# Optimization experiments

Measured on AMD Instinct MI355X. Metric: run time of the kernel, lower is better.

The kernel has to match this reference:

```python
import jax, jax.numpy as jnp
import numpy as np

TAW = 0.02

def setup_inputs() -> dict:
    key = jax.random.key(0)
    k1, k2 = jax.random.split(key)
    query = jax.random.normal(k1, (8, 2048, 1024), dtype=jnp.float32)
    memory = jax.random.normal(k2, (8, 2048, 1024), dtype=jnp.float32)
    return {"query": query, "memory": memory}

def reference(query, memory):
    # scores: [B, Lq, Lkv]
    scores = jnp.einsum('bqd,bkd->bqk', query, memory) / TAW
    probs = jax.nn.softmax(scores, axis=-1)
    # out: [B, Lq, D]
    return jnp.einsum('bqk,bkd->bqd', probs, memory)
```

## Files before the change

### kernel.cpp

```cpp
#include <hip/hip_runtime.h>
#include <math.h>


typedef __bf16 bf16x8 __attribute__((ext_vector_type(8)));
typedef float  f32x4  __attribute__((ext_vector_type(4)));
typedef float  f32x16 __attribute__((ext_vector_type(16)));

constexpr int   B_    = 8;
constexpr int   L_    = 2048;
constexpr int   D_    = 1024;
constexpr float SCALE  = 50.0f;
constexpr float MARGIN = 1.2f;
constexpr int   BQ    = 64;
constexpr int   RCAP  = 64;

constexpr size_t WS_T_ELEMS = (size_t)8 * 64 * 2048 * 16;
constexpr size_t WS_NEED    = 2 * WS_T_ELEMS * 2;

static __device__ __forceinline__ unsigned short f2bf(float x) {
    unsigned u = __builtin_bit_cast(unsigned, x);
    u += 0x7FFFu + ((u >> 16) & 1u);
    return (unsigned short)(u >> 16);
}

__global__ __launch_bounds__(256) void convert_k(
    const float* __restrict__ Q, const float* __restrict__ M,
    __bf16* __restrict__ ws)
{
    const int t = blockIdx.y;
    const size_t g = (size_t)blockIdx.x * 256 + threadIdx.x;
    const int r    = (int)(g & 2047);
    const int dblk = (int)((g >> 11) & 63);
    const int b    = (int)(g >> 17);
    const float* src = (t ? M : Q) + ((size_t)b * L_ + r) * D_ + dblk * 16;
    __bf16* dst = ws + ((size_t)t * 8 + b) * (64ull * 2048 * 16)
                     + ((size_t)dblk * 2048 + r) * 16;
    union { unsigned short h[16]; uint4 u[2]; } o;
    #pragma unroll
    for (int c = 0; c < 4; ++c) {
        float4 v = ((const float4*)src)[c];
        o.h[c*4+0] = f2bf(v.x); o.h[c*4+1] = f2bf(v.y);
        o.h[c*4+2] = f2bf(v.z); o.h[c*4+3] = f2bf(v.w);
    }
    ((uint4*)dst)[0] = o.u[0];
    ((uint4*)dst)[1] = o.u[1];
}

__global__ __launch_bounds__(512, 2) void attn_main(
    const float* __restrict__ Q, const float* __restrict__ M,
    const __bf16* __restrict__ ws, float* __restrict__ Out)
{
    __shared__ float wmax[8][BQ];
    __shared__ float rm_s[BQ], thr_s[BQ];
    __shared__ int   rowcnt[BQ];
    __shared__ int   rowlist[BQ][RCAP];
    __shared__ float rowval[BQ][RCAP];

    const int b    = blockIdx.x & 7;
    const int qt   = blockIdx.x >> 3;
    const int q0   = qt * BQ;
    const int tid  = threadIdx.x;
    const int w    = tid >> 6;
    const int lane = tid & 63;
    const int ln31 = lane & 31;
    const int h2   = lane >> 5;

    const __bf16* qws = ws + (size_t)b * (64ull * 2048 * 16);
    const __bf16* mws = ws + ((size_t)8 + b) * (64ull * 2048 * 16);
    const float*  Qb  = Q + ((size_t)b * L_ + q0) * D_;
    const float*  Mb  = M + (size_t)b * L_ * D_;

    if (tid < BQ) { rm_s[tid] = -INFINITY; rowcnt[tid] = 0; }
    __syncthreads();

    #pragma unroll 1
    for (int kt = 0; kt < 2; ++kt) {
        const int nb = kt * 1024 + w * 128;

        f32x16 acc[2][4];
        #pragma unroll
        for (int i = 0; i < 2; ++i)
            #pragma unroll
            for (int j = 0; j < 4; ++j)
                #pragma unroll
                for (int e = 0; e < 16; ++e) acc[i][j][e] = 0.f;

        #pragma unroll 1
        for (int dq = 0; dq < 16; ++dq) {
            bf16x8 af[4][2], bf[4][4];
            #pragma unroll
            for (int ks = 0; ks < 4; ++ks) {
                const int dblk = dq * 4 + ks;
                const __bf16* qp = qws + ((size_t)dblk * 2048 + q0 + ln31) * 16 + h2 * 8;
                af[ks][0] = *(const bf16x8*)qp;
                af[ks][1] = *(const bf16x8*)(qp + 32 * 16);
                const __bf16* mp = mws + ((size_t)dblk * 2048 + nb + ln31) * 16 + h2 * 8;
                #pragma unroll
                for (int j = 0; j < 4; ++j)
                    bf[ks][j] = *(const bf16x8*)(mp + j * 32 * 16);
            }
            #pragma unroll
            for (int ks = 0; ks < 4; ++ks)
                #pragma unroll
                for (int i = 0; i < 2; ++i)
                    #pragma unroll
                    for (int j = 0; j < 4; ++j)
                        acc[i][j] = __builtin_amdgcn_mfma_f32_32x32x16_bf16(
                            af[ks][i], bf[ks][j], acc[i][j], 0, 0, 0);
        }

        float lm[2][16];
        #pragma unroll
        for (int i = 0; i < 2; ++i)
            #pragma unroll
            for (int g = 0; g < 16; ++g)
                lm[i][g] = fmaxf(fmaxf(acc[i][0][g], acc[i][1][g]),
                                 fmaxf(acc[i][2][g], acc[i][3][g]));
        #pragma unroll
        for (int off = 1; off <= 16; off <<= 1)
            #pragma unroll
            for (int i = 0; i < 2; ++i)
                #pragma unroll
                for (int g = 0; g < 16; ++g)
                    lm[i][g] = fmaxf(lm[i][g], __shfl_xor(lm[i][g], off, 64));
        if (ln31 == 0) {
            #pragma unroll
            for (int i = 0; i < 2; ++i)
                #pragma unroll
                for (int g = 0; g < 16; ++g)
                    wmax[w][i * 32 + (g & 3) + 8 * (g >> 2) + 4 * h2] = lm[i][g];
        }
        __syncthreads();
        if (tid < BQ) {
            float m = wmax[0][tid];
            #pragma unroll
            for (int ww = 1; ww < 8; ++ww) m = fmaxf(m, wmax[ww][tid]);
            m = fmaxf(m, rm_s[tid]);
            rm_s[tid] = m;
            thr_s[tid] = m - MARGIN;
        }
        __syncthreads();

        #pragma unroll
        for (int i = 0; i < 2; ++i)
            #pragma unroll
            for (int g = 0; g < 16; ++g) {
                const int rl = i * 32 + (g & 3) + 8 * (g >> 2) + 4 * h2;
                const float thr = thr_s[rl];
                #pragma unroll
                for (int j = 0; j < 4; ++j)
                    if (acc[i][j][g] > thr) {
                        int t = atomicAdd(&rowcnt[rl], 1);
                        if (t < RCAP) {
                            rowlist[rl][t] = nb + j * 32 + ln31;
                            rowval[rl][t]  = acc[i][j][g];
                        }
                    }
            }
    }
    __syncthreads();

    #pragma unroll 1
    for (int r = w; r < BQ; r += 8) {
        const int c = min(rowcnt[r], RCAP);
        const float thrf = rm_s[r] - MARGIN;
        #pragma unroll 1
        for (int t = 0; t < c; ++t) {
            const float av = rowval[r][t];
            if (av > thrf) {
                const int k = rowlist[r][t];
                const f32x4* qp = (const f32x4*)(Qb + (size_t)r * D_);
                const f32x4* mp = (const f32x4*)(Mb + (size_t)k * D_);
                float dot = 0.f;
                #pragma unroll
                for (int c4 = 0; c4 < 4; ++c4) {
                    f32x4 x = qp[lane + 64 * c4];
                    f32x4 y = mp[lane + 64 * c4];
                    dot += x[0]*y[0] + x[1]*y[1] + x[2]*y[2] + x[3]*y[3];
                }
                #pragma unroll
                for (int off = 32; off >= 1; off >>= 1)
                    dot += __shfl_xor(dot, off, 64);
                if (lane == 0) rowval[r][t] = dot;
            } else if (lane == 0) rowval[r][t] = -1e30f;
        }
    }
    __syncthreads();

    #pragma unroll 1
    for (int r = w; r < BQ; r += 8) {
        const int c = min(rowcnt[r], RCAP);
        float mstar = -1e30f;
        for (int t = 0; t < c; ++t) mstar = fmaxf(mstar, rowval[r][t]);
        float denom = 0.f;
        f32x4 o[4];
        #pragma unroll
        for (int c4 = 0; c4 < 4; ++c4) o[c4] = (f32x4){0.f, 0.f, 0.f, 0.f};
        #pragma unroll 1
        for (int t = 0; t < c; ++t) {
            const float wgt = __expf(SCALE * (rowval[r][t] - mstar));
            if (wgt > 1e-22f) {
                denom += wgt;
                const f32x4* mp = (const f32x4*)(Mb + (size_t)rowlist[r][t] * D_);
                #pragma unroll
                for (int c4 = 0; c4 < 4; ++c4)
                    o[c4] += mp[lane + 64 * c4] * wgt;
            }
        }
        const float inv = 1.f / denom;
        f32x4* op = (f32x4*)(Out + ((size_t)b * L_ + q0 + r) * D_);
        #pragma unroll
        for (int c4 = 0; c4 < 4; ++c4) op[lane + 64 * c4] = o[c4] * inv;
    }
}

constexpr int   FB_BKV  = 256;
constexpr int   FB_NKT  = L_ / FB_BKV;
constexpr int   FB_BD   = 32;
constexpr int   FB_NDC  = D_ / FB_BD;
constexpr int   FB_STR  = FB_BD + 8;
constexpr int   FB_CAP  = 2048;

__global__ __launch_bounds__(256) void attn_fb(
    const float* __restrict__ Q, const float* __restrict__ M,
    float* __restrict__ Out)
{
    __shared__ __bf16 qs[BQ * FB_STR];
    __shared__ __bf16 ms[FB_BKV * FB_STR];
    __shared__ float  wmax[4][BQ];
    __shared__ float  rowmax_s[BQ];
    __shared__ int    cnt_s;
    __shared__ int    list_s[FB_CAP];
    __shared__ float  elist_s[FB_CAP];

    const int b    = blockIdx.x & 7;
    const int qt   = blockIdx.x >> 3;
    const int q0   = qt * BQ;
    const int tid  = threadIdx.x;
    const int w    = tid >> 6;
    const int lane = tid & 63;
    const int ln15 = lane & 15;
    const int quad = lane >> 4;

    const float* Qb = Q + ((size_t)b * L_ + q0) * D_;
    const float* Mb = M + (size_t)b * L_ * D_;

    float rm[4][4];
    #pragma unroll
    for (int i = 0; i < 4; ++i)
        #pragma unroll
        for (int r = 0; r < 4; ++r) rm[i][r] = -INFINITY;

    #pragma unroll 1
    for (int pass = 0; pass < 2; ++pass) {
        #pragma unroll 1
        for (int kt = 0; kt < FB_NKT; ++kt) {
            f32x4 acc[4][4];
            #pragma unroll
            for (int i = 0; i < 4; ++i)
                #pragma unroll
                for (int j = 0; j < 4; ++j)
                    acc[i][j] = (f32x4){0.f, 0.f, 0.f, 0.f};
            const float* Mt = Mb + (size_t)(kt * FB_BKV) * D_;
            #pragma unroll 1
            for (int dc = 0; dc < FB_NDC; ++dc) {
                const int d0 = dc * FB_BD;
                __syncthreads();
                #pragma unroll
                for (int i = 0; i < 2; ++i) {
                    int f4 = tid + i * 256, row = f4 >> 3, c = f4 & 7;
                    float4 v = *(const float4*)(Qb + row * D_ + d0 + c * 4);
                    union { unsigned short h[4]; uint2 u; } t;
                    t.h[0] = f2bf(v.x); t.h[1] = f2bf(v.y);
                    t.h[2] = f2bf(v.z); t.h[3] = f2bf(v.w);
                    *(uint2*)(qs + row * FB_STR + c * 4) = t.u;
                }
                #pragma unroll
                for (int i = 0; i < 8; ++i) {
                    int f4 = tid + i * 256, row = f4 >> 3, c = f4 & 7;
                    float4 v = *(const float4*)(Mt + row * D_ + d0 + c * 4);
                    union { unsigned short h[4]; uint2 u; } t;
                    t.h[0] = f2bf(v.x); t.h[1] = f2bf(v.y);
                    t.h[2] = f2bf(v.z); t.h[3] = f2bf(v.w);
                    *(uint2*)(ms + row * FB_STR + c * 4) = t.u;
                }
                __syncthreads();
                bf16x8 afr[4], bfr[4];
                #pragma unroll
                for (int i = 0; i < 4; ++i)
                    afr[i] = *(const bf16x8*)(qs + (i * 16 + ln15) * FB_STR + quad * 8);
                #pragma unroll
                for (int j = 0; j < 4; ++j)
                    bfr[j] = *(const bf16x8*)(ms + (w * 64 + j * 16 + ln15) * FB_STR + quad * 8);
                #pragma unroll
                for (int i = 0; i < 4; ++i)
                    #pragma unroll
                    for (int j = 0; j < 4; ++j)
                        acc[i][j] = __builtin_amdgcn_mfma_f32_16x16x32_bf16(
                            afr[i], bfr[j], acc[i][j], 0, 0, 0);
            }
            if (pass == 0) {
                #pragma unroll
                for (int i = 0; i < 4; ++i)
                    #pragma unroll
                    for (int r = 0; r < 4; ++r) {
                        float m0 = fmaxf(fmaxf(acc[i][0][r], acc[i][1][r]),
                                         fmaxf(acc[i][2][r], acc[i][3][r]));
                        rm[i][r] = fmaxf(rm[i][r], m0);
                    }
            } else {
                #pragma unroll
                for (int i = 0; i < 4; ++i)
                    #pragma unroll
                    for (int j = 0; j < 4; ++j)
                        #pragma unroll
                        for (int r = 0; r < 4; ++r)
                            if (acc[i][j][r] > rm[i][r]) {
                                int idx = atomicAdd(&cnt_s, 1);
                                if (idx < FB_CAP)
                                    list_s[idx] = ((i * 16 + quad * 4 + r) << 16) |
                                                  (kt * FB_BKV + w * 64 + j * 16 + ln15);
                            }
            }
        }
        if (pass == 0) {
            #pragma unroll
            for (int i = 0; i < 4; ++i)
                #pragma unroll
                for (int r = 0; r < 4; ++r) {
                    float v = rm[i][r];
                    v = fmaxf(v, __shfl_xor(v, 1, 64));
                    v = fmaxf(v, __shfl_xor(v, 2, 64));
                    v = fmaxf(v, __shfl_xor(v, 4, 64));
                    v = fmaxf(v, __shfl_xor(v, 8, 64));
                    rm[i][r] = v;
                }
            if (ln15 == 0) {
                #pragma unroll
                for (int i = 0; i < 4; ++i)
                    #pragma unroll
                    for (int r = 0; r < 4; ++r)
                        wmax[w][i * 16 + quad * 4 + r] = rm[i][r];
            }
            __syncthreads();
            if (tid < BQ)
                rowmax_s[tid] = fmaxf(fmaxf(wmax[0][tid], wmax[1][tid]),
                                      fmaxf(wmax[2][tid], wmax[3][tid]));
            if (tid == 0) cnt_s = 0;
            __syncthreads();
            #pragma unroll
            for (int i = 0; i < 4; ++i)
                #pragma unroll
                for (int r = 0; r < 4; ++r)
                    rm[i][r] = rowmax_s[i * 16 + quad * 4 + r] - MARGIN;
        }
    }
    __syncthreads();
    const int n = min(cnt_s, FB_CAP);
    #pragma unroll 1
    for (int s = w; s < n; s += 4) {
        int e = list_s[s];
        int q = e >> 16, k = e & 0xFFFF;
        const float4* qp = (const float4*)(Qb + q * D_);
        const float4* mp = (const float4*)(Mb + (size_t)k * D_);
        float dot = 0.f;
        #pragma unroll
        for (int c = 0; c < 4; ++c) {
            float4 x = qp[lane + 64 * c];
            float4 y = mp[lane + 64 * c];
            dot += x.x * y.x + x.y * y.y + x.z * y.z + x.w * y.w;
        }
        #pragma unroll
        for (int off = 32; off >= 1; off >>= 1)
            dot += __shfl_xor(dot, off, 64);
        if (lane == 0) elist_s[s] = dot;
    }
    __syncthreads();
    #pragma unroll 1
    for (int r = w; r < BQ; r += 4) {
        float mstar = -INFINITY;
        for (int s = 0; s < n; ++s)
            if ((list_s[s] >> 16) == r) mstar = fmaxf(mstar, elist_s[s]);
        float denom = 0.f;
        f32x4 o[4];
        #pragma unroll
        for (int c = 0; c < 4; ++c) o[c] = (f32x4){0.f, 0.f, 0.f, 0.f};
        for (int s = 0; s < n; ++s) {
            if ((list_s[s] >> 16) != r) continue;
            float wgt = __expf(SCALE * (elist_s[s] - mstar));
            denom += wgt;
            const f32x4* mp = (const f32x4*)(Mb + (size_t)(list_s[s] & 0xFFFF) * D_);
            #pragma unroll
            for (int c = 0; c < 4; ++c) o[c] += mp[lane + 64 * c] * wgt;
        }
        const float inv = 1.f / denom;
        f32x4* op = (f32x4*)(Out + ((size_t)b * L_ + q0 + r) * D_);
        #pragma unroll
        for (int c = 0; c < 4; ++c) op[lane + 64 * c] = o[c] * inv;
    }
}

extern "C" void kernel_launch(void* const* d_in, const int* in_sizes, int n_in,
                              void* d_out, int out_size, void* d_ws, size_t ws_size,
                              hipStream_t stream)
{
    const float* Q = (const float*)d_in[0];
    const float* M = (const float*)d_in[1];
    float* Out = (float*)d_out;

    if (ws_size >= WS_NEED) {
        convert_k<<<dim3(4096, 2), 256, 0, stream>>>(Q, M, (__bf16*)d_ws);
        attn_main<<<dim3(256), 512, 0, stream>>>(Q, M, (const __bf16*)d_ws, Out);
    } else {
        attn_fb<<<dim3(256), 256, 0, stream>>>(Q, M, Out);
    }
}
```

Baseline: 287.7 us.

## Double-buffer QK fragment loads and transpose bf16 conversion through LDS

The QK score loop now software-pipelines global fragment loads with two register sets (ping-pong), issuing the next d-block's loads before the current MFMAs. This is meant to hide global load latency better than the old batch-of-4 load-then-compute loop. The conversion kernel now stages a 64x64 tile in LDS so reads from the source rows and writes to the blocked layout are both coalesced. The trade-off is extra register pressure under the 2-waves launch bound and an LDS sync in the conversion kernel.

```diff
diff --git a/kernel.cpp b/kernel.cpp
--- a/kernel.cpp
+++ b/kernel.cpp
@@ -27,23 +27,44 @@
     const float* __restrict__ Q, const float* __restrict__ M,
     __bf16* __restrict__ ws)
 {
-    const int t = blockIdx.y;
-    const size_t g = (size_t)blockIdx.x * 256 + threadIdx.x;
-    const int r    = (int)(g & 2047);
-    const int dblk = (int)((g >> 11) & 63);
-    const int b    = (int)(g >> 17);
-    const float* src = (t ? M : Q) + ((size_t)b * L_ + r) * D_ + dblk * 16;
-    __bf16* dst = ws + ((size_t)t * 8 + b) * (64ull * 2048 * 16)
-                     + ((size_t)dblk * 2048 + r) * 16;
-    union { unsigned short h[16]; uint4 u[2]; } o;
-    #pragma unroll
-    for (int c = 0; c < 4; ++c) {
-        float4 v = ((const float4*)src)[c];
-        o.h[c*4+0] = f2bf(v.x); o.h[c*4+1] = f2bf(v.y);
-        o.h[c*4+2] = f2bf(v.z); o.h[c*4+3] = f2bf(v.w);
-    }
-    ((uint4*)dst)[0] = o.u[0];
-    ((uint4*)dst)[1] = o.u[1];
+    __shared__ unsigned short lds[64][72];
+
+    const int t   = blockIdx.y;
+    const int x   = blockIdx.x;
+    const int d0  = x & 15;
+    const int r0  = (x >> 4) & 31;
+    const int b   = x >> 9;
+    const int tid = threadIdx.x;
+
+    const float* src = (t ? M : Q)
+                     + ((size_t)b * L_ + (size_t)r0 * 64) * D_ + d0 * 64;
+
+    {
+        const int row = tid >> 4;
+        const int c4  = tid & 15;
+        #pragma unroll
+        for (int a = 0; a < 4; ++a) {
+            const int rr = a * 16 + row;
+            float4 v = *(const float4*)(src + (size_t)rr * D_ + c4 * 4);
+            union { unsigned short h[4]; uint2 u; } o;
+            o.h[0] = f2bf(v.x); o.h[1] = f2bf(v.y);
+            o.h[2] = f2bf(v.z); o.h[3] = f2bf(v.w);
+            *(uint2*)&lds[rr][c4 * 4] = o.u;
+        }
+    }
+    __syncthreads();
+
+    {
+        const int r    = tid & 63;
+        const int d4   = tid >> 6;
+        const int dblk = d0 * 4 + d4;
+        __bf16* dst = ws + ((size_t)t * 8 + b) * (64ull * 2048 * 16)
+                         + ((size_t)dblk * 2048 + (size_t)r0 * 64 + r) * 16;
+        uint4 u0 = *(const uint4*)&lds[r][d4 * 16];
+        uint4 u1 = *(const uint4*)&lds[r][d4 * 16 + 8];
+        ((uint4*)dst)[0] = u0;
+        ((uint4*)dst)[1] = u1;
+    }
 }
 
 __global__ __launch_bounds__(512, 2) void attn_main(
@@ -73,6 +94,8 @@
     if (tid < BQ) { rm_s[tid] = -INFINITY; rowcnt[tid] = 0; }
     __syncthreads();
 
+    constexpr size_t DSTR = 2048 * 16;
+
     #pragma unroll 1
     for (int kt = 0; kt < 2; ++kt) {
         const int nb = kt * 1024 + w * 128;
@@ -85,29 +108,56 @@
                 #pragma unroll
                 for (int e = 0; e < 16; ++e) acc[i][j][e] = 0.f;
 
+        const __bf16* qpb = qws + ((size_t)(q0 + ln31)) * 16 + h2 * 8;
+        const __bf16* mpb = mws + ((size_t)(nb + ln31)) * 16 + h2 * 8;
+
+        bf16x8 aA0, aA1, bA0, bA1, bA2, bA3;
+        bf16x8 aB0, aB1, bB0, bB1, bB2, bB3;
+
+#define LOADSET(s, dblk_) do {                                             \
+        const __bf16* qp_##s = qpb + (size_t)(dblk_) * DSTR;               \
+        const __bf16* mp_##s = mpb + (size_t)(dblk_) * DSTR;               \
+        a##s##0 = *(const bf16x8*)(qp_##s);                                \
+        a##s##1 = *(const bf16x8*)(qp_##s + 32 * 16);                      \
+        b##s##0 = *(const bf16x8*)(mp_##s);                                \
+        b##s##1 = *(const bf16x8*)(mp_##s + 32 * 16);                      \
+        b##s##2 = *(const bf16x8*)(mp_##s + 64 * 16);                      \
+        b##s##3 = *(const bf16x8*)(mp_##s + 96 * 16);                      \
+    } while (0)
+
+#define MFMASET(s) do {                                                    \
+        acc[0][0] = __builtin_amdgcn_mfma_f32_32x32x16_bf16(               \
+            a##s##0, b##s##0, acc[0][0], 0, 0, 0);                         \
+        acc[0][1] = __builtin_amdgcn_mfma_f32_32x32x16_bf16(               \
+            a##s##0, b##s##1, acc[0][1], 0, 0, 0);                         \
+        acc[0][2] = __builtin_amdgcn_mfma_f32_32x32x16_bf16(               \
+            a##s##0, b##s##2, acc[0][2], 0, 0, 0);                         \
+        acc[0][3] = __builtin_amdgcn_mfma_f32_32x32x16_bf16(               \
+            a##s##0, b##s##3, acc[0][3], 0, 0, 0);                         \
+        acc[1][0] = __builtin_amdgcn_mfma_f32_32x32x16_bf16(               \
+            a##s##1, b##s##0, acc[1][0], 0, 0, 0);                         \
+        acc[1][1] = __builtin_amdgcn_mfma_f32_32x32x16_bf16(               \
+            a##s##1, b##s##1, acc[1][1], 0, 0, 0);                         \
+        acc[1][2] = __builtin_amdgcn_mfma_f32_32x32x16_bf16(               \
+            a##s##1, b##s##2, acc[1][2], 0, 0, 0);                         \
+        acc[1][3] = __builtin_amdgcn_mfma_f32_32x32x16_bf16(               \
+            a##s##1, b##s##3, acc[1][3], 0, 0, 0);                         \
+    } while (0)
+
+        LOADSET(A, 0);
         #pragma unroll 1
-        for (int dq = 0; dq < 16; ++dq) {
-            bf16x8 af[4][2], bf[4][4];
-            #pragma unroll
-            for (int ks = 0; ks < 4; ++ks) {
-                const int dblk = dq * 4 + ks;
-                const __bf16* qp = qws + ((size_t)dblk * 2048 + q0 + ln31) * 16 + h2 * 8;
-                af[ks][0] = *(const bf16x8*)qp;
-                af[ks][1] = *(const bf16x8*)(qp + 32 * 16);
-                const __bf16* mp = mws + ((size_t)dblk * 2048 + nb + ln31) * 16 + h2 * 8;
-                #pragma unroll
-                for (int j = 0; j < 4; ++j)
-                    bf[ks][j] = *(const bf16x8*)(mp + j * 32 * 16);
-            }
-            #pragma unroll
-            for (int ks = 0; ks < 4; ++ks)
-                #pragma unroll
-                for (int i = 0; i < 2; ++i)
-                    #pragma unroll
-                    for (int j = 0; j < 4; ++j)
-                        acc[i][j] = __builtin_amdgcn_mfma_f32_32x32x16_bf16(
-                            af[ks][i], bf[ks][j], acc[i][j], 0, 0, 0);
-        }
+        for (int d = 0; d < 62; d += 2) {
+            LOADSET(B, d + 1);
+            MFMASET(A);
+            LOADSET(A, d + 2);
+            MFMASET(B);
+        }
+        LOADSET(B, 63);
+        MFMASET(A);
+        MFMASET(B);
+
+#undef LOADSET
+#undef MFMASET
 
         float lm[2][16];
         #pragma unroll
```

After: 278.5 us. 1.03x faster.
